# Kernel optimization log

Hardware: AMD Instinct MI355X
Metric: run time of the kernel (lower is better)

The kernel has to match this reference:

```python
import jax, jax.numpy as jnp
import numpy as np

N = 100000      # nodes
E = 1600000     # edges
F_IN = 256      # input_size
H = 64          # hidden_channels
B = 4096        # join_index batch


def gcn_conv(x, W, b, src, dst, ew, n):
    """PyG GCNConv: x' = D^-1/2 (A + I) D^-1/2 (x W) + b, with edge weights."""
    xw = x @ W  # [n, out]
    # add self-loops with weight 1
    loop = jnp.arange(n)
    src_f = jnp.concatenate([src, loop])
    dst_f = jnp.concatenate([dst, loop])
    ew_f = jnp.concatenate([ew, jnp.ones((n,), xw.dtype)])
    deg = jax.ops.segment_sum(ew_f, dst_f, num_segments=n)  # in-degree w/ self-loops
    dis = jnp.where(deg > 0, jax.lax.rsqrt(deg), 0.0)       # deg^-1/2
    norm = dis[src_f] * ew_f * dis[dst_f]                   # [E+n]
    msgs = norm[:, None] * xw[src_f]                        # gather + scale
    out = jax.ops.segment_sum(msgs, dst_f, num_segments=n)  # scatter-add
    return out + b


def setup_inputs() -> dict:
    key = jax.random.key(0)
    ks = jax.random.split(key, 10)
    x = jax.random.normal(ks[0], (N, F_IN), dtype=jnp.float32)
    edge_index = jax.random.randint(ks[1], (2, E), 0, N, dtype=jnp.int32)
    edge_col = jax.random.uniform(ks[2], (E,), dtype=jnp.float32)
    join_index = jax.random.randint(ks[3], (B,), 0, N, dtype=jnp.int32)
    # parameters (glorot-ish scaling)
    W1 = jax.random.normal(ks[4], (F_IN, H), jnp.float32) / np.sqrt(F_IN)
    b1 = jnp.zeros((H,), jnp.float32)
    W2 = jax.random.normal(ks[5], (H, 2 * H), jnp.float32) / np.sqrt(H)
    b2 = jnp.zeros((2 * H,), jnp.float32)
    Wl = jax.random.normal(ks[6], (2 * H, 1), jnp.float32) / np.sqrt(2 * H)
    bl = jnp.zeros((1,), jnp.float32)
    return {"x": x, "edge_index": edge_index, "join_index": join_index,
            "edge_col": edge_col, "W1": W1, "b1": b1, "W2": W2, "b2": b2,
            "Wl": Wl, "bl": bl}


def reference(x, edge_index, join_index, edge_col, W1, b1, W2, b2, Wl, bl):
    src, dst = edge_index[0], edge_index[1]
    h = gcn_conv(x, W1, b1, src, dst, edge_col, N)
    h = jax.nn.relu(h)
    h = gcn_conv(h, W2, b2, src, dst, edge_col, N)
    # dropout is identity in eval mode
    out = h[join_index] @ Wl + bl  # [B, 1]
    return jax.nn.sigmoid(out)
```

## Files before the change

kernel.cpp:

```cpp
#include <hip/hip_runtime.h>
#include <hip/hip_bf16.h>

#define N_NODES 100000
#define N_EDGES 1600000
#define F_INPUT 256
#define H1DIM 64
#define H2DIM 128
#define BATCH 4096

typedef unsigned short ushort_t;

static __device__ __forceinline__ ushort_t f2bf(float f) {
    unsigned u = __float_as_uint(f);
    unsigned r = (u + 0x7FFFu + ((u >> 16) & 1u)) >> 16;
    return (ushort_t)r;
}

__global__ void k_deg(const int* __restrict__ dst, const float* __restrict__ ew,
                      unsigned long long* __restrict__ degp) {
    int e = blockIdx.x * blockDim.x + threadIdx.x;
    if (e >= N_EDGES) return;
    int d = dst[e];
    unsigned long long fx = (unsigned long long)(ew[e] * 4294967296.0f);
    atomicAdd(&degp[d], (1ULL << 40) | fx);
}

__global__ void k_dis(const unsigned long long* __restrict__ degp,
                      float* __restrict__ dis, int* __restrict__ cnt) {
    int n = blockIdx.x * blockDim.x + threadIdx.x;
    if (n >= N_NODES) return;
    unsigned long long p = degp[n];
    cnt[n] = (int)(p >> 40);
    float degw = (float)((double)(p & ((1ULL << 40) - 1)) * (1.0 / 4294967296.0));
    dis[n] = rsqrtf(degw + 1.0f);
}

__global__ void k_scan1(const int* __restrict__ cnt, int* __restrict__ rowptr,
                        int* __restrict__ bsums) {
    __shared__ int sh[256];
    int base = blockIdx.x * 1024;
    int t = threadIdx.x;
    int i0 = base + t * 4;
    int v[4];
#pragma unroll
    for (int j = 0; j < 4; ++j) {
        int i = i0 + j;
        v[j] = (i < N_NODES) ? cnt[i] : 0;
    }
    int s = v[0] + v[1] + v[2] + v[3];
    sh[t] = s;
    __syncthreads();
    for (int off = 1; off < 256; off <<= 1) {
        int xv = (t >= off) ? sh[t - off] : 0;
        __syncthreads();
        sh[t] += xv;
        __syncthreads();
    }
    int ex = sh[t] - s;
    if (t == 255) bsums[blockIdx.x] = sh[255];
    int run = ex;
#pragma unroll
    for (int j = 0; j < 4; ++j) {
        int i = i0 + j;
        if (i < N_NODES) rowptr[i] = run;
        run += v[j];
    }
}

__global__ void k_scan2(int* __restrict__ bsums, int nb) {
    if (blockIdx.x == 0 && threadIdx.x == 0) {
        int run = 0;
        for (int i = 0; i < nb; ++i) { int v = bsums[i]; bsums[i] = run; run += v; }
    }
}

__global__ void k_scan3(int* __restrict__ rowptr, const int* __restrict__ bsums,
                        int* __restrict__ woff) {
    int i = blockIdx.x * blockDim.x + threadIdx.x;
    if (i == 0) rowptr[N_NODES] = N_EDGES;
    if (i >= N_NODES) return;
    int v = rowptr[i] + bsums[i >> 10];
    rowptr[i] = v;
    woff[i] = v;
}

__global__ void k_fill(const int* __restrict__ src, const int* __restrict__ dst,
                       const float* __restrict__ ew, const float* __restrict__ dis,
                       int* __restrict__ woff, int2* __restrict__ erec) {
    int e = blockIdx.x * blockDim.x + threadIdx.x;
    if (e >= N_EDGES) return;
    int s = src[e], d = dst[e];
    int pos = atomicAdd(&woff[d], 1);
    float nr = dis[s] * ew[e] * dis[d];
    erec[pos] = make_int2(s, __float_as_int(nr));
}

__global__ __launch_bounds__(256) void k_gemm1(const float* __restrict__ x,
                                               const float* __restrict__ W1,
                                               ushort_t* __restrict__ xw1b) {
    __shared__ float Ws[32 * H1DIM];
    __shared__ float As[32][68];
    int t = threadIdx.x;
    int r0 = blockIdx.x * 64;
    float acc[4][4] = {};
    int tr = t >> 4, tc = t & 15;
    for (int kc = 0; kc < 8; ++kc) {
        __syncthreads();
        for (int q = t; q < (32 * H1DIM) / 4; q += 256) {
            *(float4*)&Ws[q * 4] = *(const float4*)&W1[kc * 32 * H1DIM + q * 4];
        }
        for (int q = t; q < 512; q += 256) {
            int row = q >> 3, kg = (q & 7) * 4;
            int gr = r0 + row;
            float4 v = make_float4(0.f, 0.f, 0.f, 0.f);
            if (gr < N_NODES)
                v = *(const float4*)&x[(size_t)gr * F_INPUT + kc * 32 + kg];
            As[kg + 0][row] = v.x; As[kg + 1][row] = v.y;
            As[kg + 2][row] = v.z; As[kg + 3][row] = v.w;
        }
        __syncthreads();
#pragma unroll
        for (int k = 0; k < 32; ++k) {
            float4 a = *(float4*)&As[k][tr * 4];
            float4 b = *(float4*)&Ws[k * H1DIM + tc * 4];
            float av[4] = {a.x, a.y, a.z, a.w};
            float bv[4] = {b.x, b.y, b.z, b.w};
#pragma unroll
            for (int i = 0; i < 4; ++i)
#pragma unroll
                for (int j = 0; j < 4; ++j)
                    acc[i][j] = fmaf(av[i], bv[j], acc[i][j]);
        }
    }
#pragma unroll
    for (int i = 0; i < 4; ++i) {
        int r = r0 + tr * 4 + i;
        if (r < N_NODES) {
            ushort4 o;
            o.x = f2bf(acc[i][0]); o.y = f2bf(acc[i][1]);
            o.z = f2bf(acc[i][2]); o.w = f2bf(acc[i][3]);
            *(ushort4*)&xw1b[(size_t)r * H1DIM + tc * 4] = o;
        }
    }
}

__global__ __launch_bounds__(256) void k_agg1(const ushort_t* __restrict__ xw1b,
                                              const float* __restrict__ dis,
                                              const int* __restrict__ rowptr,
                                              const int2* __restrict__ erec,
                                              const float* __restrict__ b1,
                                              float* __restrict__ h1) {
    int wave = threadIdx.x >> 6, lane = threadIdx.x & 63;
    int n = blockIdx.x * 4 + wave;
    if (n >= N_NODES) return;
    int q = lane >> 4, ql = lane & 15;
    float a0 = 0.f, a1 = 0.f, a2 = 0.f, a3 = 0.f;
    int beg = rowptr[n], end = rowptr[n + 1];
    int E = end - beg;
    if (q == 0) {
        float dn = dis[n];
        float m = dn * dn;
        uint2 u = *(const uint2*)&xw1b[(size_t)n * H1DIM + ql * 4];
        a0 = fmaf(m, __uint_as_float(u.x << 16), a0);
        a1 = fmaf(m, __uint_as_float(u.x & 0xFFFF0000u), a1);
        a2 = fmaf(m, __uint_as_float(u.y << 16), a2);
        a3 = fmaf(m, __uint_as_float(u.y & 0xFFFF0000u), a3);
    }
    int e = q;
    for (; e + 4 < E; e += 8) {
        int2 r0 = erec[beg + e];
        int2 r1 = erec[beg + e + 4];
        uint2 u0 = *(const uint2*)&xw1b[(size_t)r0.x * H1DIM + ql * 4];
        uint2 u1 = *(const uint2*)&xw1b[(size_t)r1.x * H1DIM + ql * 4];
        float m0 = __int_as_float(r0.y), m1 = __int_as_float(r1.y);
        a0 = fmaf(m0, __uint_as_float(u0.x << 16), a0);
        a1 = fmaf(m0, __uint_as_float(u0.x & 0xFFFF0000u), a1);
        a2 = fmaf(m0, __uint_as_float(u0.y << 16), a2);
        a3 = fmaf(m0, __uint_as_float(u0.y & 0xFFFF0000u), a3);
        a0 = fmaf(m1, __uint_as_float(u1.x << 16), a0);
        a1 = fmaf(m1, __uint_as_float(u1.x & 0xFFFF0000u), a1);
        a2 = fmaf(m1, __uint_as_float(u1.y << 16), a2);
        a3 = fmaf(m1, __uint_as_float(u1.y & 0xFFFF0000u), a3);
    }
    if (e < E) {
        int2 r0 = erec[beg + e];
        uint2 u0 = *(const uint2*)&xw1b[(size_t)r0.x * H1DIM + ql * 4];
        float m0 = __int_as_float(r0.y);
        a0 = fmaf(m0, __uint_as_float(u0.x << 16), a0);
        a1 = fmaf(m0, __uint_as_float(u0.x & 0xFFFF0000u), a1);
        a2 = fmaf(m0, __uint_as_float(u0.y << 16), a2);
        a3 = fmaf(m0, __uint_as_float(u0.y & 0xFFFF0000u), a3);
    }
    a0 += __shfl_xor(a0, 16); a0 += __shfl_xor(a0, 32);
    a1 += __shfl_xor(a1, 16); a1 += __shfl_xor(a1, 32);
    a2 += __shfl_xor(a2, 16); a2 += __shfl_xor(a2, 32);
    a3 += __shfl_xor(a3, 16); a3 += __shfl_xor(a3, 32);
    if (q == 0) {
        float4 o;
        o.x = fmaxf(a0 + b1[ql * 4 + 0], 0.f);
        o.y = fmaxf(a1 + b1[ql * 4 + 1], 0.f);
        o.z = fmaxf(a2 + b1[ql * 4 + 2], 0.f);
        o.w = fmaxf(a3 + b1[ql * 4 + 3], 0.f);
        *(float4*)&h1[(size_t)n * H1DIM + ql * 4] = o;
    }
}

__global__ __launch_bounds__(256) void k_gemm2(const float* __restrict__ h1,
                                               const float* __restrict__ W2,
                                               float* __restrict__ xw2) {
    __shared__ float Ws[H1DIM * H2DIM];
    __shared__ float As[64][68];
    int t = threadIdx.x;
    int r0 = blockIdx.x * 64;
    for (int q = t; q < (H1DIM * H2DIM) / 4; q += 256) {
        *(float4*)&Ws[q * 4] = *(const float4*)&W2[q * 4];
    }
    for (int q = t; q < 1024; q += 256) {
        int row = q >> 4, kg = (q & 15) * 4;
        int gr = r0 + row;
        float4 v = make_float4(0.f, 0.f, 0.f, 0.f);
        if (gr < N_NODES)
            v = *(const float4*)&h1[(size_t)gr * H1DIM + kg];
        As[kg + 0][row] = v.x; As[kg + 1][row] = v.y;
        As[kg + 2][row] = v.z; As[kg + 3][row] = v.w;
    }
    __syncthreads();
    float acc[4][8] = {};
    int tr = t >> 4, tc = t & 15;
#pragma unroll 8
    for (int k = 0; k < 64; ++k) {
        float4 a = *(float4*)&As[k][tr * 4];
        float4 b0 = *(float4*)&Ws[k * H2DIM + tc * 8];
        float4 b1v = *(float4*)&Ws[k * H2DIM + tc * 8 + 4];
        float av[4] = {a.x, a.y, a.z, a.w};
        float bv[8] = {b0.x, b0.y, b0.z, b0.w, b1v.x, b1v.y, b1v.z, b1v.w};
#pragma unroll
        for (int i = 0; i < 4; ++i)
#pragma unroll
            for (int j = 0; j < 8; ++j)
                acc[i][j] = fmaf(av[i], bv[j], acc[i][j]);
    }
#pragma unroll
    for (int i = 0; i < 4; ++i) {
        int r = r0 + tr * 4 + i;
        if (r < N_NODES) {
            float4 v0 = make_float4(acc[i][0], acc[i][1], acc[i][2], acc[i][3]);
            float4 v1 = make_float4(acc[i][4], acc[i][5], acc[i][6], acc[i][7]);
            *(float4*)&xw2[(size_t)r * H2DIM + tc * 8] = v0;
            *(float4*)&xw2[(size_t)r * H2DIM + tc * 8 + 4] = v1;
        }
    }
}

__global__ __launch_bounds__(256) void k_agg2(const float* __restrict__ xw2,
                                              const float* __restrict__ dis,
                                              const int* __restrict__ rowptr,
                                              const int2* __restrict__ erec,
                                              const float* __restrict__ b2,
                                              const int* __restrict__ join,
                                              const float* __restrict__ Wl,
                                              const float* __restrict__ bl,
                                              float* __restrict__ out) {
    int wave = threadIdx.x >> 6, lane = threadIdx.x & 63;
    int j = blockIdx.x * 4 + wave;
    if (j >= BATCH) return;
    int n = join[j];
    float dn = dis[n];
    float a0 = dn * dn * xw2[(size_t)n * H2DIM + lane];
    float a1 = dn * dn * xw2[(size_t)n * H2DIM + 64 + lane];
    int beg = rowptr[n], end = rowptr[n + 1];
    for (int i = beg; i < end; ++i) {
        int2 r = erec[i];
        float m = __int_as_float(r.y);
        a0 = fmaf(m, xw2[(size_t)r.x * H2DIM + lane], a0);
        a1 = fmaf(m, xw2[(size_t)r.x * H2DIM + 64 + lane], a1);
    }
    a0 += b2[lane];
    a1 += b2[64 + lane];
    float p = a0 * Wl[lane] + a1 * Wl[64 + lane];
#pragma unroll
    for (int off = 32; off > 0; off >>= 1) p += __shfl_xor(p, off);
    if (lane == 0) out[j] = 1.0f / (1.0f + expf(-(p + bl[0])));
}

extern "C" void kernel_launch(void* const* d_in, const int* in_sizes, int n_in,
                              void* d_out, int out_size, void* d_ws, size_t ws_size,
                              hipStream_t stream) {
    const float* x   = (const float*)d_in[0];
    const int*   ei  = (const int*)d_in[1];
    const int*   jix = (const int*)d_in[2];
    const float* ew  = (const float*)d_in[3];
    const float* W1  = (const float*)d_in[4];
    const float* b1  = (const float*)d_in[5];
    const float* W2  = (const float*)d_in[6];
    const float* b2  = (const float*)d_in[7];
    const float* Wl  = (const float*)d_in[8];
    const float* bl  = (const float*)d_in[9];
    float* out = (float*)d_out;
    const int* srcp = ei;
    const int* dstp = ei + N_EDGES;

    char* p = (char*)d_ws;
    auto alloc = [&](size_t bytes) {
        char* r = p;
        p += (bytes + 255) & ~(size_t)255;
        return r;
    };
    unsigned long long* degp = (unsigned long long*)alloc((size_t)N_NODES * 8);
    float* dis      = (float*)alloc((size_t)N_NODES * 4);
    int*   cnt      = (int*)alloc((size_t)(N_NODES + 1) * 4);
    int*   rowptr   = (int*)alloc((size_t)(N_NODES + 1) * 4);
    int*   bsums    = (int*)alloc(1024 * 4);
    int2*  erec     = (int2*)alloc((size_t)N_EDGES * 8);
    ushort_t* xw1b  = (ushort_t*)alloc((size_t)N_NODES * H1DIM * 2);
    float* h1       = (float*)alloc((size_t)N_NODES * H1DIM * 4);
    float* xw2      = (float*)alloc((size_t)N_NODES * H2DIM * 4);

    hipMemsetAsync(degp, 0, (size_t)N_NODES * 8, stream);

    k_deg<<<(N_EDGES + 255) / 256, 256, 0, stream>>>(dstp, ew, degp);
    k_dis<<<(N_NODES + 255) / 256, 256, 0, stream>>>(degp, dis, cnt);
    int nb = (N_NODES + 1023) / 1024;
    k_scan1<<<nb, 256, 0, stream>>>(cnt, rowptr, bsums);
    k_scan2<<<1, 64, 0, stream>>>(bsums, nb);
    k_scan3<<<(N_NODES + 255) / 256, 256, 0, stream>>>(rowptr, bsums, cnt );
    k_fill<<<(N_EDGES + 255) / 256, 256, 0, stream>>>(srcp, dstp, ew, dis, cnt , erec);
    k_gemm1<<<(N_NODES + 63) / 64, 256, 0, stream>>>(x, W1, xw1b);
    k_agg1<<<(N_NODES + 3) / 4, 256, 0, stream>>>(xw1b, dis, rowptr, erec, b1, h1);
    k_gemm2<<<(N_NODES + 63) / 64, 256, 0, stream>>>(h1, W2, xw2);
    k_agg2<<<(BATCH + 3) / 4, 256, 0, stream>>>(xw2, dis, rowptr, erec, b2, jix, Wl, bl, out);
}
```

Baseline: 460.7 us.

## Build CSR via two-pass bucketed counting sort instead of global atomics

Replaces the per-edge global 64-bit atomic degree accumulation and per-edge global atomic CSR fill with a two-level bucket sort. Edges are first histogrammed and scattered into 128-node buckets using block-local shared-memory atomics. Per-bucket kernels then compute degrees and place edges into their final CSR slots with shared-memory atomics. This removes scattered global atomic contention at the cost of extra kernel launches and an extra pass over an intermediate edge buffer. Degree summation now uses float atomics, whose order is nondeterministic.

```diff
diff --git a/kernel.cpp b/kernel.cpp
--- a/kernel.cpp
+++ b/kernel.cpp
@@ -8,6 +8,10 @@
 #define H2DIM 128
 #define BATCH 4096
 
+#define NB 782
+#define BSHIFT 7
+#define BNODES 128
+
 typedef unsigned short ushort_t;
 
 static __device__ __forceinline__ ushort_t f2bf(float f) {
@@ -16,23 +20,98 @@
     return (ushort_t)r;
 }
 
-__global__ void k_deg(const int* __restrict__ dst, const float* __restrict__ ew,
-                      unsigned long long* __restrict__ degp) {
-    int e = blockIdx.x * blockDim.x + threadIdx.x;
-    if (e >= N_EDGES) return;
-    int d = dst[e];
-    unsigned long long fx = (unsigned long long)(ew[e] * 4294967296.0f);
-    atomicAdd(&degp[d], (1ULL << 40) | fx);
-}
-
-__global__ void k_dis(const unsigned long long* __restrict__ degp,
-                      float* __restrict__ dis, int* __restrict__ cnt) {
-    int n = blockIdx.x * blockDim.x + threadIdx.x;
-    if (n >= N_NODES) return;
-    unsigned long long p = degp[n];
-    cnt[n] = (int)(p >> 40);
-    float degw = (float)((double)(p & ((1ULL << 40) - 1)) * (1.0 / 4294967296.0));
-    dis[n] = rsqrtf(degw + 1.0f);
+__global__ __launch_bounds__(256) void k_hist(const int* __restrict__ dst,
+                                              unsigned* __restrict__ gcnt) {
+    __shared__ unsigned h[NB];
+    int t = threadIdx.x;
+    for (int i = t; i < NB; i += 256) h[i] = 0;
+    __syncthreads();
+    const int EPB = (N_EDGES + gridDim.x - 1) / gridDim.x;
+    int b0 = blockIdx.x * EPB, b1 = min(b0 + EPB, N_EDGES);
+    for (int e = b0 + t; e < b1; e += 256)
+        atomicAdd(&h[((unsigned)dst[e]) >> BSHIFT], 1u);
+    __syncthreads();
+    for (int i = t; i < NB; i += 256)
+        if (h[i]) atomicAdd(&gcnt[i], h[i]);
+}
+
+__global__ __launch_bounds__(256) void k_bscan(const unsigned* __restrict__ gcnt,
+                                               int* __restrict__ bptr,
+                                               int* __restrict__ bcur) {
+    __shared__ int sh[256];
+    int t = threadIdx.x;
+    int i0 = t * 4;
+    int v[4];
+#pragma unroll
+    for (int j = 0; j < 4; ++j) v[j] = (i0 + j < NB) ? (int)gcnt[i0 + j] : 0;
+    int s = v[0] + v[1] + v[2] + v[3];
+    sh[t] = s;
+    __syncthreads();
+    for (int off = 1; off < 256; off <<= 1) {
+        int xv = (t >= off) ? sh[t - off] : 0;
+        __syncthreads();
+        sh[t] += xv;
+        __syncthreads();
+    }
+    int run = sh[t] - s;
+#pragma unroll
+    for (int j = 0; j < 4; ++j) {
+        int i = i0 + j;
+        if (i < NB) { bptr[i] = run; bcur[i] = run; }
+        run += v[j];
+    }
+    if (t == 255) bptr[NB] = N_EDGES;
+}
+
+__global__ __launch_bounds__(256) void k_bscatter(const int* __restrict__ src,
+                                                  const int* __restrict__ dst,
+                                                  const float* __restrict__ ew,
+                                                  int* __restrict__ bcur,
+                                                  int2* __restrict__ bes) {
+    __shared__ unsigned h[NB];
+    __shared__ int cur[NB];
+    int t = threadIdx.x;
+    for (int i = t; i < NB; i += 256) h[i] = 0;
+    __syncthreads();
+    const int EPB = (N_EDGES + gridDim.x - 1) / gridDim.x;
+    int b0 = blockIdx.x * EPB, b1 = min(b0 + EPB, N_EDGES);
+    for (int e = b0 + t; e < b1; e += 256)
+        atomicAdd(&h[((unsigned)dst[e]) >> BSHIFT], 1u);
+    __syncthreads();
+    for (int i = t; i < NB; i += 256)
+        cur[i] = h[i] ? atomicAdd(&bcur[i], (int)h[i]) : 0;
+    __syncthreads();
+    for (int e = b0 + t; e < b1; e += 256) {
+        int d = dst[e];
+        int bk = ((unsigned)d) >> BSHIFT;
+        int pos = atomicAdd(&cur[bk], 1);
+        int packed = src[e] | ((d & (BNODES - 1)) << 17);
+        bes[pos] = make_int2(packed, __float_as_int(ew[e]));
+    }
+}
+
+__global__ __launch_bounds__(256) void k_bdeg(const int* __restrict__ bptr,
+                                              const int2* __restrict__ bes,
+                                              int* __restrict__ cnt,
+                                              float* __restrict__ dis) {
+    __shared__ unsigned cntL[BNODES];
+    __shared__ float degL[BNODES];
+    int b = blockIdx.x, t = threadIdx.x;
+    if (t < BNODES) { cntL[t] = 0u; degL[t] = 0.f; }
+    __syncthreads();
+    int e0 = bptr[b], e1 = bptr[b + 1];
+    for (int e = e0 + t; e < e1; e += 256) {
+        int2 r = bes[e];
+        int dl = (r.x >> 17) & (BNODES - 1);
+        atomicAdd(&cntL[dl], 1u);
+        atomicAdd(&degL[dl], __int_as_float(r.y));
+    }
+    __syncthreads();
+    int node = b * BNODES + t;
+    if (t < BNODES && node < N_NODES) {
+        cnt[node] = (int)cntL[t];
+        dis[node] = rsqrtf(degL[t] + 1.0f);
+    }
 }
 
 __global__ void k_scan1(const int* __restrict__ cnt, int* __restrict__ rowptr,
@@ -74,25 +153,32 @@
     }
 }
 
-__global__ void k_scan3(int* __restrict__ rowptr, const int* __restrict__ bsums,
-                        int* __restrict__ woff) {
+__global__ void k_scan3(int* __restrict__ rowptr, const int* __restrict__ bsums) {
     int i = blockIdx.x * blockDim.x + threadIdx.x;
     if (i == 0) rowptr[N_NODES] = N_EDGES;
     if (i >= N_NODES) return;
-    int v = rowptr[i] + bsums[i >> 10];
-    rowptr[i] = v;
-    woff[i] = v;
-}
-
-__global__ void k_fill(const int* __restrict__ src, const int* __restrict__ dst,
-                       const float* __restrict__ ew, const float* __restrict__ dis,
-                       int* __restrict__ woff, int2* __restrict__ erec) {
-    int e = blockIdx.x * blockDim.x + threadIdx.x;
-    if (e >= N_EDGES) return;
-    int s = src[e], d = dst[e];
-    int pos = atomicAdd(&woff[d], 1);
-    float nr = dis[s] * ew[e] * dis[d];
-    erec[pos] = make_int2(s, __float_as_int(nr));
+    rowptr[i] = rowptr[i] + bsums[i >> 10];
+}
+
+__global__ __launch_bounds__(256) void k_bfinal(const int* __restrict__ bptr,
+                                                const int* __restrict__ rowptr,
+                                                const int2* __restrict__ bes,
+                                                const float* __restrict__ dis,
+                                                int2* __restrict__ erec) {
+    __shared__ int cur[BNODES];
+    int b = blockIdx.x, t = threadIdx.x;
+    int nbase = b * BNODES;
+    if (t < BNODES && nbase + t < N_NODES) cur[t] = rowptr[nbase + t];
+    __syncthreads();
+    int e0 = bptr[b], e1 = bptr[b + 1];
+    for (int e = e0 + t; e < e1; e += 256) {
+        int2 r = bes[e];
+        int s = r.x & 0x1FFFF;
+        int dl = (r.x >> 17) & (BNODES - 1);
+        float nr = dis[s] * __int_as_float(r.y) * dis[nbase + dl];
+        int pos = atomicAdd(&cur[dl], 1);
+        erec[pos] = make_int2(s, __float_as_int(nr));
+    }
 }
 
 __global__ __launch_bounds__(256) void k_gemm1(const float* __restrict__ x,
@@ -306,7 +392,10 @@
         p += (bytes + 255) & ~(size_t)255;
         return r;
     };
-    unsigned long long* degp = (unsigned long long*)alloc((size_t)N_NODES * 8);
+    unsigned* gcnt  = (unsigned*)alloc((size_t)NB * 4);
+    int*   bptr     = (int*)alloc((size_t)(NB + 1) * 4);
+    int*   bcur     = (int*)alloc((size_t)NB * 4);
+    int2*  bes      = (int2*)alloc((size_t)N_EDGES * 8);
     float* dis      = (float*)alloc((size_t)N_NODES * 4);
     int*   cnt      = (int*)alloc((size_t)(N_NODES + 1) * 4);
     int*   rowptr   = (int*)alloc((size_t)(N_NODES + 1) * 4);
@@ -316,15 +405,17 @@
     float* h1       = (float*)alloc((size_t)N_NODES * H1DIM * 4);
     float* xw2      = (float*)alloc((size_t)N_NODES * H2DIM * 4);
 
-    hipMemsetAsync(degp, 0, (size_t)N_NODES * 8, stream);
-
-    k_deg<<<(N_EDGES + 255) / 256, 256, 0, stream>>>(dstp, ew, degp);
-    k_dis<<<(N_NODES + 255) / 256, 256, 0, stream>>>(degp, dis, cnt);
+    hipMemsetAsync(gcnt, 0, (size_t)NB * 4, stream);
+
+    k_hist<<<256, 256, 0, stream>>>(dstp, gcnt);
+    k_bscan<<<1, 256, 0, stream>>>(gcnt, bptr, bcur);
+    k_bscatter<<<256, 256, 0, stream>>>(srcp, dstp, ew, bcur, bes);
+    k_bdeg<<<NB, 256, 0, stream>>>(bptr, bes, cnt, dis);
     int nb = (N_NODES + 1023) / 1024;
     k_scan1<<<nb, 256, 0, stream>>>(cnt, rowptr, bsums);
     k_scan2<<<1, 64, 0, stream>>>(bsums, nb);
-    k_scan3<<<(N_NODES + 255) / 256, 256, 0, stream>>>(rowptr, bsums, cnt );
-    k_fill<<<(N_EDGES + 255) / 256, 256, 0, stream>>>(srcp, dstp, ew, dis, cnt , erec);
+    k_scan3<<<(N_NODES + 255) / 256, 256, 0, stream>>>(rowptr, bsums);
+    k_bfinal<<<NB, 256, 0, stream>>>(bptr, rowptr, bes, dis, erec);
     k_gemm1<<<(N_NODES + 63) / 64, 256, 0, stream>>>(x, W1, xw1b);
     k_agg1<<<(N_NODES + 3) / 4, 256, 0, stream>>>(xw1b, dis, rowptr, erec, b1, h1);
     k_gemm2<<<(N_NODES + 63) / 64, 256, 0, stream>>>(h1, W2, xw2);
```

Result: faster. 404.2 us (-12.3%).
